# Optimization experiments

Hardware: AMD Instinct MI355X
Metric: run time of the kernel (lower is better)

## Reference

```python
import jax, jax.numpy as jnp
import numpy as np

N = 20000      # num nodes
E = 320000     # num edges (before self loops)
DIN = 128      # in_channels
DH = 128       # hidden channels
C = 40         # num classes


def setup_inputs() -> dict:
    key = jax.random.key(0)
    ks = jax.random.split(key, 16)
    s_in = 1.0 / np.sqrt(DIN)
    s_h = 1.0 / np.sqrt(DH)
    s_a = 1.0 / np.sqrt(2 * DH)
    return {
        "x": jax.random.normal(ks[0], (N, DIN), jnp.float32),
        "edge_index": jax.random.randint(ks[1], (2, E), 0, N),
        "norm": jax.random.uniform(ks[2], (E + N,), jnp.float32),  # Jaccard sims in [0,1]
        # layer 1 params
        "W1": jax.random.uniform(ks[3], (DIN, DH), jnp.float32, -s_in, s_in),
        "aW1": jax.random.uniform(ks[4], (2 * DH, 1), jnp.float32, -s_a, s_a),
        "ab1": jax.random.uniform(ks[5], (1,), jnp.float32, -s_a, s_a),
        "alpha1": jnp.array([0.5], jnp.float32),
        "b1": jnp.zeros((DH,), jnp.float32),
        # layer 2 params
        "W2": jax.random.uniform(ks[6], (DH, DH), jnp.float32, -s_h, s_h),
        "aW2": jax.random.uniform(ks[7], (2 * DH, 1), jnp.float32, -s_a, s_a),
        "ab2": jax.random.uniform(ks[8], (1,), jnp.float32, -s_a, s_a),
        "alpha2": jnp.array([0.5], jnp.float32),
        "b2": jnp.zeros((DH,), jnp.float32),
        # output head
        "Wout": jax.random.uniform(ks[9], (DH, C), jnp.float32, -s_h, s_h),
        "bout": jax.random.uniform(ks[10], (C,), jnp.float32, -s_h, s_h),
    }


def _gat_layer(x, src, dst, norm, W, aW, ab, alpha, bias):
    n = x.shape[0]
    h = x @ W                              # [N, DH]
    s = h[src]                             # gathered source feats [E', DH]
    t = h[dst]                             # gathered target feats [E', DH]
    # attention logit per edge -> exp(leaky_relu(.))
    e = jnp.exp(jax.nn.leaky_relu(jnp.concatenate([s, t], axis=-1) @ aW + ab,
                                  negative_slope=0.2))          # [E', 1]
    e_sum = jax.ops.segment_sum(e, dst, num_segments=n)         # softmax denom per dst node
    a = e / e_sum[dst]
    s_sim = jnp.exp(norm)[:, None]                               # [E', 1]
    s_sum = jax.ops.segment_sum(s_sim, src, num_segments=n)     # note: summed over SRC (as in original)
    sw = s_sim / s_sum[dst]                                      # but indexed by DST (as in original)
    al = jnp.clip(alpha, 1e-4, 0.9999)
    w = al * a + (1.0 - al) * sw                                 # blended edge weight [E', 1]
    out = jax.ops.segment_max(w * s, dst, num_segments=n)        # aggr='max' propagate
    return out + bias


def reference(x, edge_index, norm, W1, aW1, ab1, alpha1, b1,
              W2, aW2, ab2, alpha2, b2, Wout, bout):
    n = x.shape[0]
    loops = jnp.arange(n, dtype=edge_index.dtype)
    src = jnp.concatenate([edge_index[0], loops])   # add_self_loops
    dst = jnp.concatenate([edge_index[1], loops])
    h = jax.nn.relu(_gat_layer(x, src, dst, norm, W1, aW1, ab1, alpha1, b1))
    h = jax.nn.relu(_gat_layer(h, src, dst, norm, W2, aW2, ab2, alpha2, b2))
    return jax.nn.log_softmax(h @ Wout + bout, axis=-1)
```

## Files before the change

kernel.cpp:

```cpp
#include <hip/hip_runtime.h>
#include <math.h>

#define DHID 128
#define NCLS 40
#define ELLW 64

typedef unsigned int   u32;
typedef unsigned short u16;
using short8 = __attribute__((ext_vector_type(8))) short;
using f32x4  = __attribute__((ext_vector_type(4))) float;

__device__ __forceinline__ u16 f2bf(float f) {
  u32 u = __float_as_uint(f);
  return (u16)((u + 0x7FFFu + ((u >> 16) & 1u)) >> 16);
}
__device__ __forceinline__ float bf_lo(u32 p) { return __uint_as_float(p << 16); }
__device__ __forceinline__ float bf_hi(u32 p) { return __uint_as_float(p & 0xFFFF0000u); }

__device__ __forceinline__ short8 packbf(float4 a, float4 b) {
  short8 r;
  r[0] = (short)f2bf(a.x); r[1] = (short)f2bf(a.y);
  r[2] = (short)f2bf(a.z); r[3] = (short)f2bf(a.w);
  r[4] = (short)f2bf(b.x); r[5] = (short)f2bf(b.y);
  r[6] = (short)f2bf(b.z); r[7] = (short)f2bf(b.w);
  return r;
}

__global__ __launch_bounds__(256) void prep_kernel(
    const float* __restrict__ W1, const float* __restrict__ W2,
    u16* __restrict__ Wp1, u16* __restrict__ Wp2,
    int* __restrict__ counts, float* __restrict__ ssum,
    int* __restrict__ ovf_cnt, int N) {
  int gi = blockIdx.x * 256 + threadIdx.x;
  if (gi < N) { counts[gi] = 0; ssum[gi] = 0.f; return; }
  gi -= N;
  if (gi < 32768) {
    int layer = gi >> 14, q = gi & 16383;
    int j = q & 7, l = (q >> 3) & 63, kt = (q >> 9) & 3, ct = q >> 11;
    int k = kt * 32 + (l >> 4) * 8 + j;
    int col = ct * 16 + (l & 15);
    const float* Wsrc = layer ? W2 : W1;
    u16* Wdst = layer ? Wp2 : Wp1;
    Wdst[q] = f2bf(Wsrc[k * DHID + col]);
    return;
  }
  gi -= 32768;
  if (gi == 0) *ovf_cnt = 0;
}

template <bool BF16IN>
__device__ __forceinline__ void mfma_gemm_block(
    float* Cl, float* P, const float* __restrict__ Xf,
    const u16* __restrict__ Xh, const u16* __restrict__ Wp,
    const float* __restrict__ aW, u16* __restrict__ Hout,
    float* __restrict__ elo, float* __restrict__ ero, int n, int rowBase) {
  int t = threadIdx.x;
  int w = t >> 6, l = t & 63;
  int lr = l & 15, lh = l >> 4;
  f32x4 acc00 = {0.f,0.f,0.f,0.f}, acc01 = {0.f,0.f,0.f,0.f};
  f32x4 acc10 = {0.f,0.f,0.f,0.f}, acc11 = {0.f,0.f,0.f,0.f};
  int r0 = rowBase + lr;      if (r0 > n - 1) r0 = n - 1;
  int r1 = rowBase + 16 + lr; if (r1 > n - 1) r1 = n - 1;
  const u16* wb0 = Wp + ((size_t)(w * 2 + 0) * 4 * 64 + l) * 8;
  const u16* wb1 = Wp + ((size_t)(w * 2 + 1) * 4 * 64 + l) * 8;
#pragma unroll
  for (int kt = 0; kt < 4; ++kt) {
    int ko = kt * 32 + lh * 8;
    short8 fa0, fa1;
    if constexpr (BF16IN) {
      fa0 = *reinterpret_cast<const short8*>(Xh + (size_t)r0 * DHID + ko);
      fa1 = *reinterpret_cast<const short8*>(Xh + (size_t)r1 * DHID + ko);
    } else {
      const float* a0f = Xf + (size_t)r0 * DHID + ko;
      const float* a1f = Xf + (size_t)r1 * DHID + ko;
      fa0 = packbf(*reinterpret_cast<const float4*>(a0f),
                   *reinterpret_cast<const float4*>(a0f + 4));
      fa1 = packbf(*reinterpret_cast<const float4*>(a1f),
                   *reinterpret_cast<const float4*>(a1f + 4));
    }
    short8 fb0 = *reinterpret_cast<const short8*>(wb0 + kt * 64 * 8);
    short8 fb1 = *reinterpret_cast<const short8*>(wb1 + kt * 64 * 8);
    acc00 = __builtin_amdgcn_mfma_f32_16x16x32_bf16(fa0, fb0, acc00, 0, 0, 0);
    acc01 = __builtin_amdgcn_mfma_f32_16x16x32_bf16(fa0, fb1, acc01, 0, 0, 0);
    acc10 = __builtin_amdgcn_mfma_f32_16x16x32_bf16(fa1, fb0, acc10, 0, 0, 0);
    acc11 = __builtin_amdgcn_mfma_f32_16x16x32_bf16(fa1, fb1, acc11, 0, 0, 0);
  }
#pragma unroll
  for (int j = 0; j < 4; ++j) {
    Cl[(lh * 4 + j) * DHID + w * 32 + lr]           = acc00[j];
    Cl[(lh * 4 + j) * DHID + w * 32 + 16 + lr]      = acc01[j];
    Cl[(16 + lh * 4 + j) * DHID + w * 32 + lr]      = acc10[j];
    Cl[(16 + lh * 4 + j) * DHID + w * 32 + 16 + lr] = acc11[j];
  }
  __syncthreads();
  int r = t >> 3, cg2 = (t & 7) * 16;
  const float* crow = Cl + r * DHID + cg2;
  float pl = 0.f, pr = 0.f;
  int gr = rowBase + r;
#pragma unroll
  for (int q = 0; q < 16; ++q) {
    float v = crow[q];
    pl = fmaf(v, aW[cg2 + q], pl);
    pr = fmaf(v, aW[DHID + cg2 + q], pr);
  }
  if (gr < n) {
    uint4 o;
    o.x = (u32)f2bf(crow[0])  | ((u32)f2bf(crow[1])  << 16);
    o.y = (u32)f2bf(crow[2])  | ((u32)f2bf(crow[3])  << 16);
    o.z = (u32)f2bf(crow[4])  | ((u32)f2bf(crow[5])  << 16);
    o.w = (u32)f2bf(crow[6])  | ((u32)f2bf(crow[7])  << 16);
    *reinterpret_cast<uint4*>(Hout + (size_t)gr * DHID + cg2) = o;
    uint4 o2;
    o2.x = (u32)f2bf(crow[8])  | ((u32)f2bf(crow[9])  << 16);
    o2.y = (u32)f2bf(crow[10]) | ((u32)f2bf(crow[11]) << 16);
    o2.z = (u32)f2bf(crow[12]) | ((u32)f2bf(crow[13]) << 16);
    o2.w = (u32)f2bf(crow[14]) | ((u32)f2bf(crow[15]) << 16);
    *reinterpret_cast<uint4*>(Hout + (size_t)gr * DHID + cg2 + 8) = o2;
  }
  P[r * 16 + (t & 7) * 2 + 0] = pl;
  P[r * 16 + (t & 7) * 2 + 1] = pr;
  __syncthreads();
  if (t < 64) {
    int half = t >> 5, rr = t & 31;
    float s = 0.f;
#pragma unroll
    for (int cq = 0; cq < 8; ++cq) s += P[rr * 16 + cq * 2 + half];
    int g2 = rowBase + rr;
    if (g2 < n) { if (half) ero[g2] = s; else elo[g2] = s; }
  }
}

__global__ __launch_bounds__(256) void gemm1_build_kernel(
    const float* __restrict__ X, const u16* __restrict__ Wp,
    const float* __restrict__ aW, u16* __restrict__ H,
    float* __restrict__ el, float* __restrict__ er, int n, int gT,
    const int* __restrict__ ei, const float* __restrict__ norm,
    int* __restrict__ counts, float* __restrict__ ssum,
    uint2* __restrict__ ell, uint4* __restrict__ ovf,
    int* __restrict__ ovf_cnt, int E, int EP) {
  __shared__ float Cl[32 * DHID];
  __shared__ float P[32 * 16];
  if (blockIdx.x < gT) {
    mfma_gemm_block<false>(Cl, P, X, nullptr, Wp, aW, H, el, er, n,
                           blockIdx.x * 32);
  } else {
    int k = (blockIdx.x - gT) * 256 + threadIdx.x;
    if (k < EP) {
      int src, dst;
      if (k < E) { src = ei[k]; dst = ei[E + k]; }
      else       { src = dst = k - E; }
      float se = __expf(norm[k]);
      atomicAdd(&ssum[src], se);
      int slot = atomicAdd(&counts[dst], 1);
      if (slot < ELLW) {
        ell[(size_t)dst * ELLW + slot] =
            make_uint2((u32)src, __float_as_uint(se));
      } else {
        int o = atomicAdd(ovf_cnt, 1);
        ovf[o] = make_uint4((u32)dst, (u32)src, __float_as_uint(se), 0u);
      }
    }
  }
}

__global__ __launch_bounds__(256) void gemm_elr_kernel(
    const u16* __restrict__ Xbf, const u16* __restrict__ Wp,
    const float* __restrict__ aW, u16* __restrict__ H,
    float* __restrict__ el, float* __restrict__ er, int n) {
  __shared__ float Cl[32 * DHID];
  __shared__ float P[32 * 16];
  mfma_gemm_block<true>(Cl, P, nullptr, Xbf, Wp, aW, H, el, er, n,
                        blockIdx.x * 32);
}

__device__ __forceinline__ void agg_node8(
    const u16* __restrict__ H, const int* __restrict__ counts,
    const uint2* __restrict__ ell, const uint4* __restrict__ ovf, int ovfN,
    const float* __restrict__ el, const float* __restrict__ ssum,
    float base, float al, int node, int lane, float a[8]) {
  int deg = counts[node];
  int dell = deg < ELLW ? deg : ELLW;
  const uint2* erow = ell + (size_t)node * ELLW;
  int src0 = 0; float sx0 = 0.f;
  if (lane < dell) {
    uint2 rec = erow[lane];
    src0 = (int)rec.x;
    sx0  = __uint_as_float(rec.y);
  }
  int qw = lane >> 4;
  const u16* Hf = H + ((lane & 15) << 3);
  int ei0 = qw, ei1 = 4 + qw;
  int ci0 = ei0 < dell ? ei0 : 0;
  int ci1 = ei1 < dell ? ei1 : 0;
  int ps0 = __shfl(src0, ci0);
  int ps1 = __shfl(src0, ci1);
  uint4 pr0 = *reinterpret_cast<const uint4*>(Hf + (size_t)ps0 * DHID);
  uint4 pr1 = *reinterpret_cast<const uint4*>(Hf + (size_t)ps1 * DHID);
  float e0 = 0.f;
  if (lane < dell) {
    float g = el[src0] + base;
    e0 = __expf(g > 0.f ? g : 0.2f * g);
  }
  float es = e0;
  if (ovfN > 0 && deg > ELLW) {
    for (int cb = 0; cb < ovfN; cb += 64) {
      int i = cb + lane;
      if (i < ovfN) {
        uint4 r = ovf[i];
        if ((int)r.x == node) {
          float g = el[(int)r.y] + base;
          es += __expf(g > 0.f ? g : 0.2f * g);
        }
      }
    }
  }
#pragma unroll
  for (int off = 32; off; off >>= 1) es += __shfl_xor(es, off);
  float invEs = al / es;
  float omaS  = (1.f - al) / ssum[node];
  float w0 = e0 * invEs + sx0 * omaS;
#pragma unroll
  for (int i = 0; i < 8; ++i) a[i] = -INFINITY;
  {
    float wA = __shfl(w0, ci0);
    float wB = __shfl(w0, ci1);
    if (ei0 < dell) {
      a[0] = fmaxf(a[0], wA * bf_lo(pr0.x)); a[1] = fmaxf(a[1], wA * bf_hi(pr0.x));
      a[2] = fmaxf(a[2], wA * bf_lo(pr0.y)); a[3] = fmaxf(a[3], wA * bf_hi(pr0.y));
      a[4] = fmaxf(a[4], wA * bf_lo(pr0.z)); a[5] = fmaxf(a[5], wA * bf_hi(pr0.z));
      a[6] = fmaxf(a[6], wA * bf_lo(pr0.w)); a[7] = fmaxf(a[7], wA * bf_hi(pr0.w));
    }
    if (ei1 < dell) {
      a[0] = fmaxf(a[0], wB * bf_lo(pr1.x)); a[1] = fmaxf(a[1], wB * bf_hi(pr1.x));
      a[2] = fmaxf(a[2], wB * bf_lo(pr1.y)); a[3] = fmaxf(a[3], wB * bf_hi(pr1.y));
      a[4] = fmaxf(a[4], wB * bf_lo(pr1.z)); a[5] = fmaxf(a[5], wB * bf_hi(pr1.z));
      a[6] = fmaxf(a[6], wB * bf_lo(pr1.w)); a[7] = fmaxf(a[7], wB * bf_hi(pr1.w));
    }
  }
  int j = 8;
  for (; j + 7 < dell; j += 8) {
    int ea = j + qw, eb = j + 4 + qw;
    int   sa = __shfl(src0, ea); float wa = __shfl(w0, ea);
    int   sb = __shfl(src0, eb); float wb = __shfl(w0, eb);
    uint4 ha = *reinterpret_cast<const uint4*>(Hf + (size_t)sa * DHID);
    uint4 hb = *reinterpret_cast<const uint4*>(Hf + (size_t)sb * DHID);
    a[0] = fmaxf(a[0], fmaxf(wa * bf_lo(ha.x), wb * bf_lo(hb.x)));
    a[1] = fmaxf(a[1], fmaxf(wa * bf_hi(ha.x), wb * bf_hi(hb.x)));
    a[2] = fmaxf(a[2], fmaxf(wa * bf_lo(ha.y), wb * bf_lo(hb.y)));
    a[3] = fmaxf(a[3], fmaxf(wa * bf_hi(ha.y), wb * bf_hi(hb.y)));
    a[4] = fmaxf(a[4], fmaxf(wa * bf_lo(ha.z), wb * bf_lo(hb.z)));
    a[5] = fmaxf(a[5], fmaxf(wa * bf_hi(ha.z), wb * bf_hi(hb.z)));
    a[6] = fmaxf(a[6], fmaxf(wa * bf_lo(ha.w), wb * bf_lo(hb.w)));
    a[7] = fmaxf(a[7], fmaxf(wa * bf_hi(ha.w), wb * bf_hi(hb.w)));
  }
  for (; j < dell; j += 4) {
    int e = j + qw;
    int ec = e < dell ? e : dell - 1;
    int   sa = __shfl(src0, ec); float wa = __shfl(w0, ec);
    if (e < dell) {
      uint4 ha = *reinterpret_cast<const uint4*>(Hf + (size_t)sa * DHID);
      a[0] = fmaxf(a[0], wa * bf_lo(ha.x));
      a[1] = fmaxf(a[1], wa * bf_hi(ha.x));
      a[2] = fmaxf(a[2], wa * bf_lo(ha.y));
      a[3] = fmaxf(a[3], wa * bf_hi(ha.y));
      a[4] = fmaxf(a[4], wa * bf_lo(ha.z));
      a[5] = fmaxf(a[5], wa * bf_hi(ha.z));
      a[6] = fmaxf(a[6], wa * bf_lo(ha.w));
      a[7] = fmaxf(a[7], wa * bf_hi(ha.w));
    }
  }
  if (ovfN > 0 && deg > ELLW) {
    for (int cb = 0; cb < ovfN; cb += 64) {
      int i = cb + lane;
      uint4 r = (i < ovfN) ? ovf[i] : make_uint4(0u, 0u, 0u, 0u);
      bool match = (i < ovfN) && ((int)r.x == node);
      int si = (int)r.y;
      float wi = 0.f;
      if (match) {
        float g = el[si] + base;
        wi = __expf(g > 0.f ? g : 0.2f * g) * invEs +
             __uint_as_float(r.z) * omaS;
      }
      unsigned long long mask = __ballot(match);
      while (mask) {
        int jb = __ffsll(mask) - 1;
        mask &= mask - 1;
        int   sj = __shfl(si, jb);
        float wj = __shfl(wi, jb);
        uint4 h = *reinterpret_cast<const uint4*>(Hf + (size_t)sj * DHID);
        a[0] = fmaxf(a[0], wj * bf_lo(h.x)); a[1] = fmaxf(a[1], wj * bf_hi(h.x));
        a[2] = fmaxf(a[2], wj * bf_lo(h.y)); a[3] = fmaxf(a[3], wj * bf_hi(h.y));
        a[4] = fmaxf(a[4], wj * bf_lo(h.z)); a[5] = fmaxf(a[5], wj * bf_hi(h.z));
        a[6] = fmaxf(a[6], wj * bf_lo(h.w)); a[7] = fmaxf(a[7], wj * bf_hi(h.w));
      }
    }
  }
#pragma unroll
  for (int i = 0; i < 8; ++i) {
    a[i] = fmaxf(a[i], __shfl_xor(a[i], 16));
    a[i] = fmaxf(a[i], __shfl_xor(a[i], 32));
  }
}

__global__ __launch_bounds__(256) void agg_kernel(
    const u16* __restrict__ H, const int* __restrict__ counts,
    const uint2* __restrict__ ell, const uint4* __restrict__ ovf,
    const int* __restrict__ ovf_cnt, const float* __restrict__ el,
    const float* __restrict__ er, const float* __restrict__ ssum,
    const float* __restrict__ ab, const float* __restrict__ alpha,
    const float* __restrict__ bias, u16* __restrict__ Y, int n) {
  int node = blockIdx.x * 4 + (threadIdx.x >> 6);
  int lane = threadIdx.x & 63;
  if (node >= n) return;
  int ovfN = *ovf_cnt;
  float al = fminf(fmaxf(alpha[0], 1e-4f), 0.9999f);
  float base = er[node] + ab[0];
  float a[8];
  agg_node8(H, counts, ell, ovf, ovfN, el, ssum, base, al, node, lane, a);
  if (lane < 16) {
    int fl = lane << 3;
    float v[8];
#pragma unroll
    for (int i = 0; i < 8; ++i) v[i] = fmaxf(a[i] + bias[fl + i], 0.f);
    uint4 o;
    o.x = (u32)f2bf(v[0]) | ((u32)f2bf(v[1]) << 16);
    o.y = (u32)f2bf(v[2]) | ((u32)f2bf(v[3]) << 16);
    o.z = (u32)f2bf(v[4]) | ((u32)f2bf(v[5]) << 16);
    o.w = (u32)f2bf(v[6]) | ((u32)f2bf(v[7]) << 16);
    *reinterpret_cast<uint4*>(Y + (size_t)node * DHID + fl) = o;
  }
}

__global__ __launch_bounds__(256) void agg_head_kernel(
    const u16* __restrict__ H, const int* __restrict__ counts,
    const uint2* __restrict__ ell, const uint4* __restrict__ ovf,
    const int* __restrict__ ovf_cnt, const float* __restrict__ el,
    const float* __restrict__ er, const float* __restrict__ ssum,
    const float* __restrict__ ab, const float* __restrict__ alpha,
    const float* __restrict__ bias, const float* __restrict__ Wout,
    const float* __restrict__ bout, float* __restrict__ out, int n) {
  __shared__ float Wl[DHID * NCLS];
  __shared__ float hl[4][DHID];
  int t = threadIdx.x;
  for (int i = t; i < DHID * NCLS; i += 256) Wl[i] = Wout[i];
  int wv = t >> 6, lane = t & 63;
  int node = blockIdx.x * 4 + wv;
  if (node < n) {
    int ovfN = *ovf_cnt;
    float al = fminf(fmaxf(alpha[0], 1e-4f), 0.9999f);
    float base = er[node] + ab[0];
    float a[8];
    agg_node8(H, counts, ell, ovf, ovfN, el, ssum, base, al, node, lane, a);
    if (lane < 16) {
      int fl = lane << 3;
#pragma unroll
      for (int i = 0; i < 8; ++i)
        hl[wv][fl + i] = fmaxf(a[i] + bias[fl + i], 0.f);
    }
  }
  __syncthreads();
  if (node >= n) return;
  float z = -INFINITY;
  bool act = lane < NCLS;
  if (act) {
    z = bout[lane];
    const float* hr = hl[wv];
#pragma unroll 8
    for (int k = 0; k < DHID; ++k) z = fmaf(hr[k], Wl[k * NCLS + lane], z);
  }
  float m = z;
#pragma unroll
  for (int off = 32; off; off >>= 1) m = fmaxf(m, __shfl_xor(m, off));
  float p = act ? expf(z - m) : 0.f;
#pragma unroll
  for (int off = 32; off; off >>= 1) p += __shfl_xor(p, off);
  float ls = logf(p);
  if (act) out[(size_t)node * NCLS + lane] = z - m - ls;
}

extern "C" void kernel_launch(void* const* d_in, const int* in_sizes, int n_in,
                              void* d_out, int out_size, void* d_ws, size_t ws_size,
                              hipStream_t stream) {
  const float* x     = (const float*)d_in[0];
  const int*   ei    = (const int*)d_in[1];
  const float* norm  = (const float*)d_in[2];
  const float* W1    = (const float*)d_in[3];
  const float* aW1   = (const float*)d_in[4];
  const float* ab1   = (const float*)d_in[5];
  const float* alpha1= (const float*)d_in[6];
  const float* b1    = (const float*)d_in[7];
  const float* W2    = (const float*)d_in[8];
  const float* aW2   = (const float*)d_in[9];
  const float* ab2   = (const float*)d_in[10];
  const float* alpha2= (const float*)d_in[11];
  const float* b2    = (const float*)d_in[12];
  const float* Wout  = (const float*)d_in[13];
  const float* bout  = (const float*)d_in[14];
  float* out = (float*)d_out;

  const int N  = in_sizes[0] / DHID;
  const int E  = in_sizes[1] / 2;
  const int EP = E + N;

  char* ws = (char*)d_ws;
  size_t off = 0;
  auto alloc = [&](size_t bytes) -> void* {
    void* p = ws + off;
    off += (bytes + 255) & ~(size_t)255;
    return p;
  };
  int*   counts  = (int*)  alloc((size_t)N * 4);
  float* ssum    = (float*)alloc((size_t)N * 4);
  int*   ovf_cnt = (int*)  alloc(256);
  u16*   Wp1     = (u16*)  alloc(16384 * 2);
  u16*   Wp2     = (u16*)  alloc(16384 * 2);
  u16*   Hbf     = (u16*)  alloc((size_t)N * DHID * 2);
  u16*   Bbf     = (u16*)  alloc((size_t)N * DHID * 2);
  float* el      = (float*)alloc((size_t)N * 4);
  float* er      = (float*)alloc((size_t)N * 4);
  uint2* ell     = (uint2*)alloc((size_t)N * ELLW * 8);
  uint4* ovf     = (uint4*)alloc((size_t)EP * 16);

  const int gEdge = (EP + 255) / 256;
  const int gT    = (N + 31) / 32;
  const int gAgg  = (N + 3) / 4;
  const int prepWork = N + 32768 + 1;
  const int gPrep = (prepWork + 255) / 256;

  prep_kernel<<<gPrep, 256, 0, stream>>>(W1, W2, Wp1, Wp2,
                                         counts, ssum, ovf_cnt, N);
  gemm1_build_kernel<<<gT + gEdge, 256, 0, stream>>>(
      x, Wp1, aW1, Hbf, el, er, N, gT, ei, norm, counts, ssum, ell, ovf,
      ovf_cnt, E, EP);
  agg_kernel<<<gAgg, 256, 0, stream>>>(Hbf, counts, ell, ovf, ovf_cnt, el, er,
                                       ssum, ab1, alpha1, b1, Bbf, N);
  gemm_elr_kernel<<<gT, 256, 0, stream>>>(Bbf, Wp2, aW2, Hbf, el, er, N);
  agg_head_kernel<<<gAgg, 256, 0, stream>>>(Hbf, counts, ell, ovf, ovf_cnt,
                                            el, er, ssum, ab2, alpha2, b2,
                                            Wout, bout, out, N);
}
```

Baseline: 107.0 us.

## Split layer-1 aggregation across two feature halves per node

Replaces the layer-1 aggregation kernel with one that assigns each node to two wavefronts, each handling 64 of the 128 features. Each wave now processes 8 edges at a time with 8 lanes per edge instead of 4 edges with 16 lanes, and the block index is arranged so both halves of a node group are scheduled close together. The goal is more parallelism and more gather requests in flight per node. The cost is that edge loading, attention exponentials and the softmax denominator (including the overflow scan) are computed twice per node.

New measurement: 111.9 us. 4.6% more time.

```diff
diff --git a/kernel.cpp b/kernel.cpp
--- a/kernel.cpp
+++ b/kernel.cpp
@@ -173,6 +173,155 @@
                         blockIdx.x * 32);
 }
 
+__global__ __launch_bounds__(256) void agg1_split_kernel(
+    const u16* __restrict__ H, const int* __restrict__ counts,
+    const uint2* __restrict__ ell, const uint4* __restrict__ ovf,
+    const int* __restrict__ ovf_cnt, const float* __restrict__ el,
+    const float* __restrict__ er, const float* __restrict__ ssum,
+    const float* __restrict__ ab, const float* __restrict__ alpha,
+    const float* __restrict__ bias, u16* __restrict__ Y, int n, int ngrp) {
+  int b = blockIdx.x;
+  int pair = b >> 3, r = b & 7;
+  int h = r >> 2;
+  int g = pair * 4 + (r & 3);
+  if (g >= ngrp) return;
+  int wv = threadIdx.x >> 6, lane = threadIdx.x & 63;
+  int node = g * 4 + wv;
+  if (node >= n) return;
+
+  int ovfN = *ovf_cnt;
+  float al = fminf(fmaxf(alpha[0], 1e-4f), 0.9999f);
+  float base = er[node] + ab[0];
+
+  int deg = counts[node];
+  int dell = deg < ELLW ? deg : ELLW;
+  const uint2* erow = ell + (size_t)node * ELLW;
+  int src0 = 0; float sx0 = 0.f;
+  if (lane < dell) {
+    uint2 rec = erow[lane];
+    src0 = (int)rec.x;
+    sx0  = __uint_as_float(rec.y);
+  }
+  int eo = lane >> 3;
+  const u16* Hf = H + h * 64 + ((lane & 7) << 3);
+  int c0 = eo < dell ? eo : 0;
+  int e1 = 8 + eo;
+  int c1 = e1 < dell ? e1 : 0;
+  int ps0 = __shfl(src0, c0);
+  int ps1 = __shfl(src0, c1);
+  uint4 pr0 = *reinterpret_cast<const uint4*>(Hf + (size_t)ps0 * DHID);
+  uint4 pr1 = *reinterpret_cast<const uint4*>(Hf + (size_t)ps1 * DHID);
+  float e0 = 0.f;
+  if (lane < dell) {
+    float gl = el[src0] + base;
+    e0 = __expf(gl > 0.f ? gl : 0.2f * gl);
+  }
+  float es = e0;
+  if (ovfN > 0 && deg > ELLW) {
+    for (int cb = 0; cb < ovfN; cb += 64) {
+      int i = cb + lane;
+      if (i < ovfN) {
+        uint4 rr2 = ovf[i];
+        if ((int)rr2.x == node) {
+          float gl = el[(int)rr2.y] + base;
+          es += __expf(gl > 0.f ? gl : 0.2f * gl);
+        }
+      }
+    }
+  }
+#pragma unroll
+  for (int off = 32; off; off >>= 1) es += __shfl_xor(es, off);
+  float invEs = al / es;
+  float omaS  = (1.f - al) / ssum[node];
+  float w0 = e0 * invEs + sx0 * omaS;
+
+  float a[8];
+#pragma unroll
+  for (int i = 0; i < 8; ++i) a[i] = -INFINITY;
+  {
+    float wA = __shfl(w0, c0);
+    float wB = __shfl(w0, c1);
+    if (eo < dell) {
+      a[0] = fmaxf(a[0], wA * bf_lo(pr0.x)); a[1] = fmaxf(a[1], wA * bf_hi(pr0.x));
+      a[2] = fmaxf(a[2], wA * bf_lo(pr0.y)); a[3] = fmaxf(a[3], wA * bf_hi(pr0.y));
+      a[4] = fmaxf(a[4], wA * bf_lo(pr0.z)); a[5] = fmaxf(a[5], wA * bf_hi(pr0.z));
+      a[6] = fmaxf(a[6], wA * bf_lo(pr0.w)); a[7] = fmaxf(a[7], wA * bf_hi(pr0.w));
+    }
+    if (e1 < dell) {
+      a[0] = fmaxf(a[0], wB * bf_lo(pr1.x)); a[1] = fmaxf(a[1], wB * bf_hi(pr1.x));
+      a[2] = fmaxf(a[2], wB * bf_lo(pr1.y)); a[3] = fmaxf(a[3], wB * bf_hi(pr1.y));
+      a[4] = fmaxf(a[4], wB * bf_lo(pr1.z)); a[5] = fmaxf(a[5], wB * bf_hi(pr1.z));
+      a[6] = fmaxf(a[6], wB * bf_lo(pr1.w)); a[7] = fmaxf(a[7], wB * bf_hi(pr1.w));
+    }
+  }
+  int j = 16;
+  for (; j + 7 < dell; j += 8) {
+    int e = j + eo;
+    int   sa = __shfl(src0, e); float wa = __shfl(w0, e);
+    uint4 ha = *reinterpret_cast<const uint4*>(Hf + (size_t)sa * DHID);
+    a[0] = fmaxf(a[0], wa * bf_lo(ha.x)); a[1] = fmaxf(a[1], wa * bf_hi(ha.x));
+    a[2] = fmaxf(a[2], wa * bf_lo(ha.y)); a[3] = fmaxf(a[3], wa * bf_hi(ha.y));
+    a[4] = fmaxf(a[4], wa * bf_lo(ha.z)); a[5] = fmaxf(a[5], wa * bf_hi(ha.z));
+    a[6] = fmaxf(a[6], wa * bf_lo(ha.w)); a[7] = fmaxf(a[7], wa * bf_hi(ha.w));
+  }
+  if (j < dell) {
+    int e = j + eo;
+    int ec = e < dell ? e : dell - 1;
+    int   sa = __shfl(src0, ec); float wa = __shfl(w0, ec);
+    if (e < dell) {
+      uint4 ha = *reinterpret_cast<const uint4*>(Hf + (size_t)sa * DHID);
+      a[0] = fmaxf(a[0], wa * bf_lo(ha.x)); a[1] = fmaxf(a[1], wa * bf_hi(ha.x));
+      a[2] = fmaxf(a[2], wa * bf_lo(ha.y)); a[3] = fmaxf(a[3], wa * bf_hi(ha.y));
+      a[4] = fmaxf(a[4], wa * bf_lo(ha.z)); a[5] = fmaxf(a[5], wa * bf_hi(ha.z));
+      a[6] = fmaxf(a[6], wa * bf_lo(ha.w)); a[7] = fmaxf(a[7], wa * bf_hi(ha.w));
+    }
+  }
+  if (ovfN > 0 && deg > ELLW) {
+    for (int cb = 0; cb < ovfN; cb += 64) {
+      int i = cb + lane;
+      uint4 rr2 = (i < ovfN) ? ovf[i] : make_uint4(0u, 0u, 0u, 0u);
+      bool match = (i < ovfN) && ((int)rr2.x == node);
+      int si = (int)rr2.y;
+      float wi = 0.f;
+      if (match) {
+        float gl = el[si] + base;
+        wi = __expf(gl > 0.f ? gl : 0.2f * gl) * invEs +
+             __uint_as_float(rr2.z) * omaS;
+      }
+      unsigned long long mask = __ballot(match);
+      while (mask) {
+        int jb = __ffsll(mask) - 1;
+        mask &= mask - 1;
+        int   sj = __shfl(si, jb);
+        float wj = __shfl(wi, jb);
+        uint4 hq = *reinterpret_cast<const uint4*>(Hf + (size_t)sj * DHID);
+        a[0] = fmaxf(a[0], wj * bf_lo(hq.x)); a[1] = fmaxf(a[1], wj * bf_hi(hq.x));
+        a[2] = fmaxf(a[2], wj * bf_lo(hq.y)); a[3] = fmaxf(a[3], wj * bf_hi(hq.y));
+        a[4] = fmaxf(a[4], wj * bf_lo(hq.z)); a[5] = fmaxf(a[5], wj * bf_hi(hq.z));
+        a[6] = fmaxf(a[6], wj * bf_lo(hq.w)); a[7] = fmaxf(a[7], wj * bf_hi(hq.w));
+      }
+    }
+  }
+#pragma unroll
+  for (int i = 0; i < 8; ++i) {
+    a[i] = fmaxf(a[i], __shfl_xor(a[i], 8));
+    a[i] = fmaxf(a[i], __shfl_xor(a[i], 16));
+    a[i] = fmaxf(a[i], __shfl_xor(a[i], 32));
+  }
+  if (lane < 8) {
+    int fl = h * 64 + (lane << 3);
+    float v[8];
+#pragma unroll
+    for (int i = 0; i < 8; ++i) v[i] = fmaxf(a[i] + bias[fl + i], 0.f);
+    uint4 o;
+    o.x = (u32)f2bf(v[0]) | ((u32)f2bf(v[1]) << 16);
+    o.y = (u32)f2bf(v[2]) | ((u32)f2bf(v[3]) << 16);
+    o.z = (u32)f2bf(v[4]) | ((u32)f2bf(v[5]) << 16);
+    o.w = (u32)f2bf(v[6]) | ((u32)f2bf(v[7]) << 16);
+    *reinterpret_cast<uint4*>(Y + (size_t)node * DHID + fl) = o;
+  }
+}
+
 __device__ __forceinline__ void agg_node8(
     const u16* __restrict__ H, const int* __restrict__ counts,
     const uint2* __restrict__ ell, const uint4* __restrict__ ovf, int ovfN,
@@ -299,35 +448,6 @@
   for (int i = 0; i < 8; ++i) {
     a[i] = fmaxf(a[i], __shfl_xor(a[i], 16));
     a[i] = fmaxf(a[i], __shfl_xor(a[i], 32));
-  }
-}
-
-__global__ __launch_bounds__(256) void agg_kernel(
-    const u16* __restrict__ H, const int* __restrict__ counts,
-    const uint2* __restrict__ ell, const uint4* __restrict__ ovf,
-    const int* __restrict__ ovf_cnt, const float* __restrict__ el,
-    const float* __restrict__ er, const float* __restrict__ ssum,
-    const float* __restrict__ ab, const float* __restrict__ alpha,
-    const float* __restrict__ bias, u16* __restrict__ Y, int n) {
-  int node = blockIdx.x * 4 + (threadIdx.x >> 6);
-  int lane = threadIdx.x & 63;
-  if (node >= n) return;
-  int ovfN = *ovf_cnt;
-  float al = fminf(fmaxf(alpha[0], 1e-4f), 0.9999f);
-  float base = er[node] + ab[0];
-  float a[8];
-  agg_node8(H, counts, ell, ovf, ovfN, el, ssum, base, al, node, lane, a);
-  if (lane < 16) {
-    int fl = lane << 3;
-    float v[8];
-#pragma unroll
-    for (int i = 0; i < 8; ++i) v[i] = fmaxf(a[i] + bias[fl + i], 0.f);
-    uint4 o;
-    o.x = (u32)f2bf(v[0]) | ((u32)f2bf(v[1]) << 16);
-    o.y = (u32)f2bf(v[2]) | ((u32)f2bf(v[3]) << 16);
-    o.z = (u32)f2bf(v[4]) | ((u32)f2bf(v[5]) << 16);
-    o.w = (u32)f2bf(v[6]) | ((u32)f2bf(v[7]) << 16);
-    *reinterpret_cast<uint4*>(Y + (size_t)node * DHID + fl) = o;
   }
 }
 
@@ -424,6 +544,8 @@
   const int gEdge = (EP + 255) / 256;
   const int gT    = (N + 31) / 32;
   const int gAgg  = (N + 3) / 4;
+  const int ngrp  = (N + 3) / 4;
+  const int gAgg1 = ((ngrp + 3) / 4) * 8;
   const int prepWork = N + 32768 + 1;
   const int gPrep = (prepWork + 255) / 256;
 
@@ -432,8 +554,9 @@
   gemm1_build_kernel<<<gT + gEdge, 256, 0, stream>>>(
       x, Wp1, aW1, Hbf, el, er, N, gT, ei, norm, counts, ssum, ell, ovf,
       ovf_cnt, E, EP);
-  agg_kernel<<<gAgg, 256, 0, stream>>>(Hbf, counts, ell, ovf, ovf_cnt, el, er,
-                                       ssum, ab1, alpha1, b1, Bbf, N);
+  agg1_split_kernel<<<gAgg1, 256, 0, stream>>>(Hbf, counts, ell, ovf, ovf_cnt,
+                                               el, er, ssum, ab1, alpha1, b1,
+                                               Bbf, N, ngrp);
   gemm_elr_kernel<<<gT, 256, 0, stream>>>(Bbf, Wp2, aW2, Hbf, el, er, N);
   agg_head_kernel<<<gAgg, 256, 0, stream>>>(Hbf, counts, ell, ovf, ovf_cnt,
                                             el, er, ssum, ab2, alpha2, b2,
```
